# Kernel tuning notes

Measured on AMD Instinct MI355X. Metric: run time of the kernel, lower is better.

Reference implementation:

```python
import jax, jax.numpy as jnp
import numpy as np

N_CH = 62
B = 128
F = 32
T = 128
K = 3
HID = 512
OUT = 4
E_PER = 992


def setup_inputs() -> dict:
    key = jax.random.key(0)
    ks = jax.random.split(key, 16)
    N = B * N_CH
    E = B * E_PER
    x = jax.random.normal(ks[0], (N, F, T), dtype=jnp.float32)
    # one shared intra-graph edge pattern, offset per graph; no self-loops
    src0 = jax.random.randint(ks[1], (E_PER,), 0, N_CH)
    off = jax.random.randint(ks[2], (E_PER,), 1, N_CH)
    dst0 = (src0 + off) % N_CH
    gid = (jnp.arange(B) * N_CH)[:, None]
    src = (src0[None, :] + gid).reshape(-1)
    dst = (dst0[None, :] + gid).reshape(-1)
    edge_index = jnp.stack([src, dst]).astype(jnp.int32)
    edge_weight = jax.random.uniform(ks[3], (E,), dtype=jnp.float32, minval=0.1, maxval=1.0)
    batch = jnp.repeat(jnp.arange(B, dtype=jnp.int32), N_CH)
    sF = 1.0 / np.sqrt(F)
    sI = 1.0 / np.sqrt(N_CH * F)
    sH = 1.0 / np.sqrt(HID)
    return {
        'x': x, 'edge_index': edge_index, 'edge_weight': edge_weight, 'batch': batch,
        'W_cheb1': jax.random.normal(ks[4], (K, F, F), jnp.float32) * sF,
        'b_cheb1': jnp.zeros((F,), jnp.float32),
        'W_cheb2': jax.random.normal(ks[5], (K, F, F), jnp.float32) * sF,
        'b_cheb2': jnp.zeros((F,), jnp.float32),
        'W_ih': jax.random.normal(ks[6], (3 * HID, N_CH * F), jnp.float32) * sI,
        'W_hh': jax.random.normal(ks[7], (3 * HID, HID), jnp.float32) * sH,
        'b_ih': jnp.zeros((3 * HID,), jnp.float32),
        'b_hh': jnp.zeros((3 * HID,), jnp.float32),
        'W_lin': jax.random.normal(ks[8], (OUT, HID), jnp.float32) * sH,
        'b_lin': jnp.zeros((OUT,), jnp.float32),
    }


def _cheb_conv(x, src, dst, w, W, b):
    # PyG ChebConv, normalization='sym', lambda_max=2 => L_hat off-diag = -D^-1/2 A D^-1/2, diag 0
    N = x.shape[0]
    deg = jax.ops.segment_sum(w, src, num_segments=N)
    dinv = jnp.where(deg > 0, jax.lax.rsqrt(deg), 0.0)
    wn = -dinv[src] * w * dinv[dst]

    def prop(t):  # t: [N, F, T]
        return jax.ops.segment_sum(wn[:, None, None] * t[src], dst, num_segments=N)

    Tx0 = x
    out = jnp.einsum('nft,fg->ngt', Tx0, W[0])
    Tx1 = prop(Tx0)
    out = out + jnp.einsum('nft,fg->ngt', Tx1, W[1])
    for k in range(2, W.shape[0]):
        Tx2 = 2.0 * prop(Tx1) - Tx0
        out = out + jnp.einsum('nft,fg->ngt', Tx2, W[k])
        Tx0, Tx1 = Tx1, Tx2
    return out + b[None, :, None]


def _gru(seq, W_ih, W_hh, b_ih, b_hh):  # seq: [B, T, D]
    xg = jnp.einsum('btd,gd->btg', seq, W_ih) + b_ih  # [B, T, 3H] input gates precomputed
    h0 = jnp.zeros((seq.shape[0], W_hh.shape[1]), seq.dtype)

    def step(h, xg_t):
        hg = h @ W_hh.T + b_hh
        xr, xz, xn = jnp.split(xg_t, 3, axis=-1)
        hr, hz, hn = jnp.split(hg, 3, axis=-1)
        r = jax.nn.sigmoid(xr + hr)
        z = jax.nn.sigmoid(xz + hz)
        n = jnp.tanh(xn + r * hn)
        return (1.0 - z) * n + z * h, None

    hT, _ = jax.lax.scan(step, h0, jnp.swapaxes(xg, 0, 1))
    return hT  # [B, H]


def reference(x, edge_index, edge_weight, batch, W_cheb1, b_cheb1, W_cheb2, b_cheb2,
              W_ih, W_hh, b_ih, b_hh, W_lin, b_lin):
    src, dst = edge_index[0], edge_index[1]
    h = jax.nn.leaky_relu(_cheb_conv(x, src, dst, edge_weight, W_cheb1, b_cheb1), 0.01)
    h = _cheb_conv(h, src, dst, edge_weight, W_cheb2, b_cheb2)  # [N, F, T]
    nb = h.shape[0] // N_CH
    h = h.reshape(nb, N_CH * h.shape[1], h.shape[2])  # [B, 62F, T]
    h = jnp.swapaxes(h, 1, 2)  # [B, T, 62F]
    hid = _gru(h, W_ih, W_hh, b_ih, b_hh)  # dropout is identity (eval / p=0)
    return hid @ W_lin.T + b_lin
```

## Files before the change

kernel.cpp:

```cpp
#include <hip/hip_runtime.h>
#include <math.h>

#define N_CH 62
#define NB 128
#define F 32
#define TLEN 128
#define HID 512
#define G3 1536
#define EPER 992
#define NNODE (N_CH * NB)
#define ETOT (EPER * NB)
#define DIM (N_CH * F)
#define MROWS (NB * TLEN)
#define GRU_BLOCKS 16

typedef __attribute__((ext_vector_type(8))) short bf16x8;
typedef __attribute__((ext_vector_type(4))) float f32x4;

__device__ __forceinline__ unsigned short f2bf(float f) {
  unsigned u = __float_as_uint(f);
  unsigned r = u + 0x7fffu + ((u >> 16) & 1u);
  return (unsigned short)(r >> 16);
}
__device__ __forceinline__ float bf2f(unsigned short u) {
  return __uint_as_float(((unsigned)u) << 16);
}
__device__ __forceinline__ float sigmoidf_(float x) { return 1.f / (1.f + __expf(-x)); }

__device__ __forceinline__ void gl_lds16(const void* g, void* l) {
  __builtin_amdgcn_global_load_lds(
      (const __attribute__((address_space(1))) unsigned int*)g,
      (__attribute__((address_space(3))) unsigned int*)l, 16, 0, 0);
}

__global__ void k_deg(const int* __restrict__ src, const float* __restrict__ w,
                      float* __restrict__ deg) {
  int e = blockIdx.x * 256 + threadIdx.x;
  if (e < ETOT) atomicAdd(&deg[src[e]], w[e]);
}

__global__ void k_wn(const int* __restrict__ src, const int* __restrict__ dst,
                     const float* __restrict__ w, const float* __restrict__ deg,
                     float* __restrict__ wn) {
  int e = blockIdx.x * 256 + threadIdx.x;
  if (e < ETOT) {
    float ds = deg[src[e]], dd = deg[dst[e]];
    float a = ds > 0.f ? rsqrtf(ds) : 0.f;
    float b = dd > 0.f ? rsqrtf(dd) : 0.f;
    wn[e] = -a * w[e] * b;
  }
}

__global__ void k_ldense(const int* __restrict__ src, const int* __restrict__ dst,
                         const float* __restrict__ wn, float* __restrict__ Lf) {
  int e = blockIdx.x * 256 + threadIdx.x;
  if (e < ETOT) {
    int b = e / EPER;
    int s = src[e] - b * N_CH;
    int d = dst[e] - b * N_CH;
    atomicAdd(&Lf[(size_t)b * 4096 + d * 64 + s], wn[e]);
  }
}

__global__ __launch_bounds__(256) void k_m2(const float* __restrict__ Lf,
                                            unsigned short* __restrict__ Lbf,
                                            unsigned short* __restrict__ M2bf) {
  int b = blockIdx.x, tid = threadIdx.x;
  __shared__ float Ls[4096];
  for (int i = tid; i < 4096; i += 256) Ls[i] = Lf[(size_t)b * 4096 + i];
  __syncthreads();
  for (int h = 0; h < 16; h++) {
    int i = h * 256 + tid;
    int d = i >> 6, s = i & 63;
    float m = 0.f;
#pragma unroll 8
    for (int k = 0; k < 64; k++) m += Ls[d * 64 + k] * Ls[k * 64 + s];
    M2bf[(size_t)b * 4096 + i] = f2bf(2.f * m - (d == s ? 1.f : 0.f));
    Lbf[(size_t)b * 4096 + i] = f2bf(Ls[i]);
  }
}

__global__ __launch_bounds__(256) void k_xt(const float* __restrict__ x,
                                            unsigned short* __restrict__ Xt0) {
  int b = blockIdx.x >> 5, f = blockIdx.x & 31;
  int tid = threadIdx.x;
  for (int u = tid; u < 1024; u += 256) {
    int t = u >> 3, ch = u & 7;
    unsigned short o[8];
#pragma unroll
    for (int j = 0; j < 8; j++) {
      int n = ch * 8 + j;
      float v = (n < N_CH) ? x[((size_t)(b * N_CH + n) * F + f) * TLEN + t] : 0.f;
      o[j] = f2bf(v);
    }
    *(uint4*)&Xt0[((size_t)b * 4096 + t * 32 + f) * 64 + ch * 8] = *(uint4*)o;
  }
}

template <int LAYER>
__global__ __launch_bounds__(256) void k_cheb(const unsigned short* __restrict__ Xt,
                                              const unsigned short* __restrict__ Lbg,
                                              const unsigned short* __restrict__ M2g,
                                              const float* __restrict__ W,
                                              const float* __restrict__ bias,
                                              void* __restrict__ outv) {
  int b = blockIdx.x >> 5, ts = blockIdx.x & 31;
  int tid = threadIdx.x;
  int wid = tid >> 6, lane = tid & 63;
  int lr = lane & 15, lk = lane >> 4;
  __shared__ unsigned short Z0[128 * 64];
  __shared__ unsigned short P1[128 * 64];
  __shared__ unsigned short P2[128 * 64];

  const size_t tile_base = ((size_t)b * 4096 + ts * 128) * 64;

#pragma unroll
  for (int h = 0; h < 4; h++) {
    int p = h * 256 + tid;
    int row = p >> 3, c = (p & 7) ^ (row & 7);
    gl_lds16(Xt + tile_base + (size_t)row * 64 + c * 8,
             &Z0[(h * 256 + wid * 64) * 8]);
  }
  __syncthreads();

  f32x4 acc1[2][4], acc2[2][4];
#pragma unroll
  for (int mt = 0; mt < 2; mt++)
#pragma unroll
    for (int nt = 0; nt < 4; nt++) {
      acc1[mt][nt] = (f32x4){0.f, 0.f, 0.f, 0.f};
      acc2[mt][nt] = (f32x4){0.f, 0.f, 0.f, 0.f};
    }
  const unsigned short* Lbb = Lbg + (size_t)b * 4096;
  const unsigned short* Mbb = M2g + (size_t)b * 4096;
#pragma unroll
  for (int kk = 0; kk < 2; kk++) {
    bf16x8 af[2];
#pragma unroll
    for (int mt = 0; mt < 2; mt++) {
      int row = wid * 32 + mt * 16 + lr;
      af[mt] = *(const bf16x8*)&Z0[row * 64 + ((((kk << 2) + lk) ^ (row & 7)) << 3)];
    }
#pragma unroll
    for (int nt = 0; nt < 4; nt++) {
      int brow = nt * 16 + lr;
      bf16x8 bL = *(const bf16x8*)&Lbb[brow * 64 + kk * 32 + lk * 8];
      bf16x8 bM = *(const bf16x8*)&Mbb[brow * 64 + kk * 32 + lk * 8];
#pragma unroll
      for (int mt = 0; mt < 2; mt++) {
        acc1[mt][nt] = __builtin_amdgcn_mfma_f32_16x16x32_bf16(af[mt], bL, acc1[mt][nt], 0, 0, 0);
        acc2[mt][nt] = __builtin_amdgcn_mfma_f32_16x16x32_bf16(af[mt], bM, acc2[mt][nt], 0, 0, 0);
      }
    }
  }
#pragma unroll
  for (int mt = 0; mt < 2; mt++)
#pragma unroll
    for (int nt = 0; nt < 4; nt++) {
      int n = nt * 16 + lr;
#pragma unroll
      for (int r = 0; r < 4; r++) {
        int row = wid * 32 + mt * 16 + lk * 4 + r;
        int elem = row * 64 + ((((n >> 3) ^ (row & 7)) << 3)) + (n & 7);
        P1[elem] = f2bf(acc1[mt][nt][r]);
        P2[elem] = f2bf(acc2[mt][nt][r]);
      }
    }
  __syncthreads();

  int tl = tid >> 6, n = tid & 63;
  float acc[32];
#pragma unroll
  for (int g = 0; g < 32; g++) acc[g] = bias[g];
#pragma unroll 4
  for (int f = 0; f < 32; f++) {
    int row = tl * 32 + f;
    int elem = row * 64 + ((((n >> 3) ^ (row & 7)) << 3)) + (n & 7);
    float z0 = bf2f(Z0[elem]);
    float p1 = bf2f(P1[elem]);
    float p2 = bf2f(P2[elem]);
#pragma unroll
    for (int g = 0; g < 32; g++) {
      acc[g] += z0 * W[f * 32 + g] + p1 * W[1024 + f * 32 + g] + p2 * W[2048 + f * 32 + g];
    }
  }

  if (LAYER == 1) {
    unsigned short* out = (unsigned short*)outv;
    unsigned short* dst = out + tile_base + (size_t)(tl * 32) * 64 + n;
#pragma unroll
    for (int g = 0; g < 32; g++) {
      float y = acc[g];
      y = y > 0.f ? y : 0.01f * y;
      dst[g * 64] = f2bf(y);
    }
  } else {
    if (n < N_CH) {
      unsigned uu[16];
#pragma unroll
      for (int q = 0; q < 16; q++)
        uu[q] = (unsigned)f2bf(acc[2 * q]) | ((unsigned)f2bf(acc[2 * q + 1]) << 16);
      unsigned short* dst = (unsigned short*)outv +
                            ((size_t)(b * TLEN + ts * 4 + tl)) * DIM + n * F;
#pragma unroll
      for (int q = 0; q < 4; q++)
        *(uint4*)(dst + q * 8) = *(uint4*)&uu[q * 4];
    }
  }
}

__global__ void k_cvt(const float* __restrict__ in, unsigned short* __restrict__ out, int n) {
  int i = (blockIdx.x * 256 + threadIdx.x) * 4;
  if (i < n) {
    float4 v = *(const float4*)&in[i];
    ushort4 o;
    o.x = f2bf(v.x); o.y = f2bf(v.y); o.z = f2bf(v.z); o.w = f2bf(v.w);
    *(ushort4*)&out[i] = o;
  }
}

__global__ __launch_bounds__(256) void k_gemm_mfma(const unsigned short* __restrict__ Aq,
                                                   const unsigned short* __restrict__ Bq,
                                                   const float* __restrict__ bias,
                                                   float* __restrict__ Cmat) {
  __shared__ unsigned short As[4096];
  __shared__ unsigned short Bs[4096];
  int tid = threadIdx.x;
  int wid = tid >> 6, lane = tid & 63;
  int lr = lane & 15, lk = lane >> 4;
  int m0 = blockIdx.x * 128, n0 = blockIdx.y * 128;
  int wm = (wid & 1) * 64, wn = (wid >> 1) * 64;
  f32x4 zero = {0.f, 0.f, 0.f, 0.f};
  f32x4 acc[4][4];
#pragma unroll
  for (int i = 0; i < 4; i++)
#pragma unroll
    for (int j = 0; j < 4; j++) acc[i][j] = zero;

  int s0 = tid, s1 = tid + 256;
  const unsigned short* ga0 = Aq + (size_t)(m0 + (s0 >> 2)) * DIM + (s0 & 3) * 8;
  const unsigned short* ga1 = Aq + (size_t)(m0 + (s1 >> 2)) * DIM + (s1 & 3) * 8;
  const unsigned short* gb0 = Bq + (size_t)(n0 + (s0 >> 2)) * DIM + (s0 & 3) * 8;
  const unsigned short* gb1 = Bq + (size_t)(n0 + (s1 >> 2)) * DIM + (s1 & 3) * 8;

  for (int k0 = 0; k0 < DIM; k0 += 32) {
    gl_lds16(ga0 + k0, &As[wid * 512]);
    gl_lds16(ga1 + k0, &As[(wid + 4) * 512]);
    gl_lds16(gb0 + k0, &Bs[wid * 512]);
    gl_lds16(gb1 + k0, &Bs[(wid + 4) * 512]);
    __syncthreads();
    bf16x8 a[4], b[4];
#pragma unroll
    for (int mi = 0; mi < 4; mi++)
      a[mi] = *(const bf16x8*)&As[(wm + mi * 16 + lr) * 32 + lk * 8];
#pragma unroll
    for (int ni = 0; ni < 4; ni++)
      b[ni] = *(const bf16x8*)&Bs[(wn + ni * 16 + lr) * 32 + lk * 8];
#pragma unroll
    for (int mi = 0; mi < 4; mi++)
#pragma unroll
      for (int ni = 0; ni < 4; ni++)
        acc[mi][ni] = __builtin_amdgcn_mfma_f32_16x16x32_bf16(a[mi], b[ni], acc[mi][ni], 0, 0, 0);
    __syncthreads();
  }

#pragma unroll
  for (int mi = 0; mi < 4; mi++)
#pragma unroll
    for (int ni = 0; ni < 4; ni++) {
      int row = m0 + wm + mi * 16 + lk * 4;
      int col = n0 + wn + ni * 16 + lr;
      float bv = bias[col];
#pragma unroll
      for (int r = 0; r < 4; r++)
        Cmat[(size_t)(row + r) * G3 + col] = acc[mi][ni][r] + bv;
    }
}

#define LDH(I, OFFS) \
  asm volatile("global_load_dwordx4 %0, %1, off offset:" OFFS " sc0 sc1" \
               : "=v"(av[I]) : "v"(hin_p));
#define STH(VAL, OFFS) \
  asm volatile("global_store_short %0, %1, off offset:" OFFS " sc0 sc1" \
               :: "v"(hout_p), "v"((unsigned)(VAL)) : "memory");

__global__ __launch_bounds__(512, 1) void k_gru_persistent(
    const float* __restrict__ xg,
    const unsigned short* __restrict__ Wb,
    const float* __restrict__ bhh,
    unsigned short* __restrict__ hbA,
    unsigned short* __restrict__ hbB,
    float* __restrict__ hf_out,
    unsigned int* __restrict__ flags) {
  __shared__ unsigned short Wlds[96 * 520];
  int tid = threadIdx.x;
  int wv = tid >> 6, lane = tid & 63;
  int lr = lane & 15, lk = lane >> 4;
  int jh0 = blockIdx.x * 32;
  int mo = wv * 16;

  for (int i = tid; i < 96 * 64; i += 512) {
    int row = i >> 6, chunk = i & 63;
    int g = row >> 5, jj = row & 31;
    bf16x8 v = *(const bf16x8*)&Wb[(size_t)(g * HID + jh0 + jj) * HID + chunk * 8];
    *(bf16x8*)&Wlds[row * 520 + chunk * 8] = v;
  }
  __syncthreads();

  float br[2], bz[2], bn[2];
#pragma unroll
  for (int a = 0; a < 2; a++) {
    int j = jh0 + a * 16 + lr;
    br[a] = bhh[j]; bz[a] = bhh[HID + j]; bn[a] = bhh[2 * HID + j];
  }

  float hm[2][4];
#pragma unroll
  for (int a = 0; a < 2; a++)
#pragma unroll
    for (int r = 0; r < 4; r++) hm[a][r] = 0.f;

  float xv[2][4][3];
#pragma unroll
  for (int a = 0; a < 2; a++) {
    int j = jh0 + a * 16 + lr;
#pragma unroll
    for (int r = 0; r < 4; r++) {
      size_t xrow = ((size_t)(mo + lk * 4 + r) * TLEN + 0) * G3;
      xv[a][r][0] = xg[xrow + j];
      xv[a][r][1] = xg[xrow + HID + j];
      xv[a][r][2] = xg[xrow + 2 * HID + j];
    }
  }

  int fidx = (lane & 15) * 16;

  for (int t = 0; t < TLEN; t++) {
    const unsigned short* hin = (t & 1) ? hbB : hbA;
    unsigned short* hout = (t & 1) ? hbA : hbB;
    const unsigned short* hin_p = hin + (size_t)(mo + lr) * HID + lk * 8;
    unsigned short* hout_p = hout + (size_t)(mo + lk * 4) * HID + jh0 + lr;

    bf16x8 av[16];
    LDH(0, "0")    LDH(1, "64")   LDH(2, "128")  LDH(3, "192")
    LDH(4, "256")  LDH(5, "320")  LDH(6, "384")  LDH(7, "448")
    LDH(8, "512")  LDH(9, "576")  LDH(10, "640") LDH(11, "704")
    LDH(12, "768") LDH(13, "832") LDH(14, "896") LDH(15, "960")
    asm volatile("s_waitcnt vmcnt(0)" ::: "memory");
    __builtin_amdgcn_sched_barrier(0);

    f32x4 acc[6];
#pragma unroll
    for (int n = 0; n < 6; n++) acc[n] = (f32x4){0.f, 0.f, 0.f, 0.f};
#pragma unroll
    for (int ks = 0; ks < 16; ks++) {
#pragma unroll
      for (int n = 0; n < 6; n++) {
        bf16x8 bv = *(const bf16x8*)&Wlds[((n >> 1) * 32 + (n & 1) * 16 + lr) * 520 + ks * 32 + lk * 8];
        acc[n] = __builtin_amdgcn_mfma_f32_16x16x32_bf16(av[ks], bv, acc[n], 0, 0, 0);
      }
    }

    unsigned hv[2][4];
#pragma unroll
    for (int a = 0; a < 2; a++) {
#pragma unroll
      for (int r = 0; r < 4; r++) {
        float rr = sigmoidf_(xv[a][r][0] + acc[a][r] + br[a]);
        float zz = sigmoidf_(xv[a][r][1] + acc[2 + a][r] + bz[a]);
        float nn = tanhf(xv[a][r][2] + rr * (acc[4 + a][r] + bn[a]));
        float hnew = (1.f - zz) * nn + zz * hm[a][r];
        hm[a][r] = hnew;
        hv[a][r] = f2bf(hnew);
      }
    }

    STH(hv[0][0], "0")    STH(hv[0][1], "1024") STH(hv[0][2], "2048") STH(hv[0][3], "3072")
    STH(hv[1][0], "32")   STH(hv[1][1], "1056") STH(hv[1][2], "2080") STH(hv[1][3], "3104")

    if (t < TLEN - 1) {
      asm volatile("s_waitcnt vmcnt(0)" ::: "memory");
      __syncthreads();
      if (tid == 0)
        __hip_atomic_store(&flags[blockIdx.x * 16], (unsigned)(t + 1),
                           __ATOMIC_RELAXED, __HIP_MEMORY_SCOPE_AGENT);

      float xn[2][4][3];
#pragma unroll
      for (int a = 0; a < 2; a++) {
        int j = jh0 + a * 16 + lr;
#pragma unroll
        for (int r = 0; r < 4; r++) {
          size_t xrow = ((size_t)(mo + lk * 4 + r) * TLEN + (t + 1)) * G3;
          xn[a][r][0] = xg[xrow + j];
          xn[a][r][1] = xg[xrow + HID + j];
          xn[a][r][2] = xg[xrow + 2 * HID + j];
        }
      }

      unsigned tgt = (unsigned)(t + 1);
      while (true) {
        unsigned v = __hip_atomic_load(&flags[fidx], __ATOMIC_RELAXED, __HIP_MEMORY_SCOPE_AGENT);
        if (__ballot(v >= tgt) == ~0ull) break;
        __builtin_amdgcn_s_sleep(0);
      }

#pragma unroll
      for (int a = 0; a < 2; a++)
#pragma unroll
        for (int r = 0; r < 4; r++) {
          xv[a][r][0] = xn[a][r][0];
          xv[a][r][1] = xn[a][r][1];
          xv[a][r][2] = xn[a][r][2];
        }
    }
  }

#pragma unroll
  for (int a = 0; a < 2; a++)
#pragma unroll
    for (int r = 0; r < 4; r++)
      hf_out[(size_t)(mo + lk * 4 + r) * HID + jh0 + a * 16 + lr] = hm[a][r];
}

__global__ void k_final(const float* __restrict__ h, const float* __restrict__ Wlin,
                        const float* __restrict__ blin, float* __restrict__ out) {
  int b = blockIdx.x;
  int tid = threadIdx.x;
  int o = tid >> 6, lane = tid & 63;
  float acc = 0.f;
  for (int k = lane; k < HID; k += 64) acc += h[(size_t)b * HID + k] * Wlin[o * HID + k];
#pragma unroll
  for (int off = 32; off; off >>= 1) acc += __shfl_down(acc, off);
  if (lane == 0) out[b * 4 + o] = acc + blin[o];
}

extern "C" void kernel_launch(void* const* d_in, const int* in_sizes, int n_in,
                              void* d_out, int out_size, void* d_ws, size_t ws_size,
                              hipStream_t stream) {
  const float* x = (const float*)d_in[0];
  const int* eidx = (const int*)d_in[1];
  const float* ew = (const float*)d_in[2];
  const float* Wc1 = (const float*)d_in[4];
  const float* bc1 = (const float*)d_in[5];
  const float* Wc2 = (const float*)d_in[6];
  const float* bc2 = (const float*)d_in[7];
  const float* Wih = (const float*)d_in[8];
  const float* Whh = (const float*)d_in[9];
  const float* bih = (const float*)d_in[10];
  const float* bhh = (const float*)d_in[11];
  const float* Wlin = (const float*)d_in[12];
  const float* blin = (const float*)d_in[13];
  const int* src = eidx;
  const int* dst = eidx + ETOT;

  char* ws = (char*)d_ws;
  unsigned short* Xt0 = (unsigned short*)ws;
  unsigned short* Xt1 = (unsigned short*)(ws + 67108864);
  unsigned short* Db  = (unsigned short*)(ws + 134217728);
  float* xg = (float*)(ws + 199229440);
  char* S = ws + 299892736;
  float* deg = (float*)S;
  float* wn = (float*)(S + 32768);
  float* Lf = (float*)(S + 540672);
  unsigned short* Lb = (unsigned short*)(S + 2637824);
  unsigned short* M2b = (unsigned short*)(S + 3686400);
  unsigned short* Wihb = (unsigned short*)(S + 4734976);
  unsigned short* Whhb = (unsigned short*)(S + 10829824);
  float* hf = (float*)(S + 12402688);
  unsigned short* hbA = (unsigned short*)(S + 12664832);
  unsigned short* hbB = (unsigned short*)(S + 12795904);
  unsigned int* flags = (unsigned int*)(S + 12926976);

  if (ws_size < 312820736) return;

  hipMemsetAsync(deg, 0, 32768, stream);
  hipMemsetAsync(Lf, 0, 2097152, stream);
  hipMemsetAsync(hbA, 0, 131072, stream);
  hipMemsetAsync(flags, 0, 1024, stream);

  k_deg<<<ETOT / 256, 256, 0, stream>>>(src, ew, deg);
  k_wn<<<ETOT / 256, 256, 0, stream>>>(src, dst, ew, deg, wn);
  k_ldense<<<ETOT / 256, 256, 0, stream>>>(src, dst, wn, Lf);
  k_m2<<<NB, 256, 0, stream>>>(Lf, Lb, M2b);
  k_xt<<<NB * 32, 256, 0, stream>>>(x, Xt0);

  k_cheb<1><<<NB * 32, 256, 0, stream>>>(Xt0, Lb, M2b, Wc1, bc1, Xt1);
  k_cheb<2><<<NB * 32, 256, 0, stream>>>(Xt1, Lb, M2b, Wc2, bc2, Db);

  k_cvt<<<(G3 * DIM / 4 + 255) / 256, 256, 0, stream>>>(Wih, Wihb, G3 * DIM);
  k_cvt<<<(G3 * HID / 4 + 255) / 256, 256, 0, stream>>>(Whh, Whhb, G3 * HID);

  dim3 gg(MROWS / 128, G3 / 128);
  k_gemm_mfma<<<gg, 256, 0, stream>>>(Db, Wihb, bih, xg);

  k_gru_persistent<<<GRU_BLOCKS, 512, 0, stream>>>(xg, Whhb, bhh, hbA, hbB, hf, flags);

  k_final<<<NB, 256, 0, stream>>>(hf, Wlin, blin, (float*)d_out);
}
```

Before: 1.766 ms.

## Replace GRU flag barrier with per-element step tags and split K polling

```diff
diff --git a/kernel.cpp b/kernel.cpp
--- a/kernel.cpp
+++ b/kernel.cpp
@@ -16,6 +16,7 @@
 
 typedef __attribute__((ext_vector_type(8))) short bf16x8;
 typedef __attribute__((ext_vector_type(4))) float f32x4;
+typedef __attribute__((ext_vector_type(4))) unsigned int u32x4;
 
 __device__ __forceinline__ unsigned short f2bf(float f) {
   unsigned u = __float_as_uint(f);
@@ -31,6 +32,15 @@
   __builtin_amdgcn_global_load_lds(
       (const __attribute__((address_space(1))) unsigned int*)g,
       (__attribute__((address_space(3))) unsigned int*)l, 16, 0, 0);
+}
+
+__device__ __forceinline__ bf16x8 pack_hi(u32x4 lo, u32x4 hi) {
+  u32x4 r;
+  r[0] = (lo[0] >> 16) | (lo[1] & 0xffff0000u);
+  r[1] = (lo[2] >> 16) | (lo[3] & 0xffff0000u);
+  r[2] = (hi[0] >> 16) | (hi[1] & 0xffff0000u);
+  r[3] = (hi[2] >> 16) | (hi[3] & 0xffff0000u);
+  return __builtin_bit_cast(bf16x8, r);
 }
 
 __global__ void k_deg(const int* __restrict__ src, const float* __restrict__ w,
@@ -84,16 +94,29 @@
                                             unsigned short* __restrict__ Xt0) {
   int b = blockIdx.x >> 5, f = blockIdx.x & 31;
   int tid = threadIdx.x;
-  for (int u = tid; u < 1024; u += 256) {
-    int t = u >> 3, ch = u & 7;
-    unsigned short o[8];
-#pragma unroll
-    for (int j = 0; j < 8; j++) {
-      int n = ch * 8 + j;
-      float v = (n < N_CH) ? x[((size_t)(b * N_CH + n) * F + f) * TLEN + t] : 0.f;
-      o[j] = f2bf(v);
-    }
-    *(uint4*)&Xt0[((size_t)b * 4096 + t * 32 + f) * 64 + ch * 8] = *(uint4*)o;
+  __shared__ unsigned short T[128 * 72];
+#pragma unroll
+  for (int h = 0; h < 8; h++) {
+    int idx = h * 256 + tid;
+    int n = idx >> 5, tq = idx & 31;
+    if (n < N_CH) {
+      float4 v = *(const float4*)&x[(((size_t)(b * N_CH + n)) * F + f) * TLEN + tq * 4];
+      T[(tq * 4 + 0) * 72 + n] = f2bf(v.x);
+      T[(tq * 4 + 1) * 72 + n] = f2bf(v.y);
+      T[(tq * 4 + 2) * 72 + n] = f2bf(v.z);
+      T[(tq * 4 + 3) * 72 + n] = f2bf(v.w);
+    } else {
+      T[(tq * 4 + 0) * 72 + n] = 0; T[(tq * 4 + 1) * 72 + n] = 0;
+      T[(tq * 4 + 2) * 72 + n] = 0; T[(tq * 4 + 3) * 72 + n] = 0;
+    }
+  }
+  __syncthreads();
+  int t = tid >> 1, half = tid & 1;
+  unsigned short* dst = &Xt0[((size_t)b * 4096 + t * 32 + f) * 64 + half * 32];
+#pragma unroll
+  for (int q = 0; q < 4; q++) {
+    uint4 v = *(const uint4*)&T[t * 72 + half * 32 + q * 8];
+    *(uint4*)(dst + q * 8) = v;
   }
 }
 
@@ -277,21 +300,35 @@
     }
 }
 
-#define LDH(I, OFFS) \
-  asm volatile("global_load_dwordx4 %0, %1, off offset:" OFFS " sc0 sc1" \
-               : "=v"(av[I]) : "v"(hin_p));
-#define STH(VAL, OFFS) \
-  asm volatile("global_store_short %0, %1, off offset:" OFFS " sc0 sc1" \
-               :: "v"(hout_p), "v"((unsigned)(VAL)) : "memory");
+#define LDK(ARR, I, OFF) \
+  asm volatile("global_load_dwordx4 %0, %1, off offset:" OFF " sc0 sc1" \
+               : "=v"(ARR[I]) : "v"(hp));
+#define LD16_0 \
+  LDK(st, 0, "0")    LDK(st, 1, "16")   LDK(st, 2, "128")  LDK(st, 3, "144") \
+  LDK(st, 4, "256")  LDK(st, 5, "272")  LDK(st, 6, "384")  LDK(st, 7, "400") \
+  LDK(st, 8, "512")  LDK(st, 9, "528")  LDK(st, 10, "640") LDK(st, 11, "656") \
+  LDK(st, 12, "768") LDK(st, 13, "784") LDK(st, 14, "896") LDK(st, 15, "912")
+#define LD16_1 \
+  LDK(st, 0, "1024") LDK(st, 1, "1040") LDK(st, 2, "1152") LDK(st, 3, "1168") \
+  LDK(st, 4, "1280") LDK(st, 5, "1296") LDK(st, 6, "1408") LDK(st, 7, "1424") \
+  LDK(st, 8, "1536") LDK(st, 9, "1552") LDK(st, 10, "1664") LDK(st, 11, "1680") \
+  LDK(st, 12, "1792") LDK(st, 13, "1808") LDK(st, 14, "1920") LDK(st, 15, "1936")
+#define STW(P, VAL, OFF) \
+  asm volatile("global_store_dword %0, %1, off offset:" OFF " sc0 sc1" \
+               :: "v"(P), "v"(VAL) : "memory");
+#define TAGCHK \
+  unsigned diff = 0; \
+  _Pragma("unroll") \
+  for (int i_ = 0; i_ < 16; i_++) \
+    diff |= (st[i_][0] ^ tag) | (st[i_][1] ^ tag) | (st[i_][2] ^ tag) | (st[i_][3] ^ tag);
 
 __global__ __launch_bounds__(512, 1) void k_gru_persistent(
     const float* __restrict__ xg,
     const unsigned short* __restrict__ Wb,
     const float* __restrict__ bhh,
-    unsigned short* __restrict__ hbA,
-    unsigned short* __restrict__ hbB,
-    float* __restrict__ hf_out,
-    unsigned int* __restrict__ flags) {
+    unsigned* __restrict__ hA,
+    unsigned* __restrict__ hB,
+    float* __restrict__ hf_out) {
   __shared__ unsigned short Wlds[96 * 520];
   int tid = threadIdx.x;
   int wv = tid >> 6, lane = tid & 63;
@@ -333,35 +370,75 @@
     }
   }
 
-  int fidx = (lane & 15) * 16;
-
   for (int t = 0; t < TLEN; t++) {
-    const unsigned short* hin = (t & 1) ? hbB : hbA;
-    unsigned short* hout = (t & 1) ? hbA : hbB;
-    const unsigned short* hin_p = hin + (size_t)(mo + lr) * HID + lk * 8;
-    unsigned short* hout_p = hout + (size_t)(mo + lk * 4) * HID + jh0 + lr;
-
-    bf16x8 av[16];
-    LDH(0, "0")    LDH(1, "64")   LDH(2, "128")  LDH(3, "192")
-    LDH(4, "256")  LDH(5, "320")  LDH(6, "384")  LDH(7, "448")
-    LDH(8, "512")  LDH(9, "576")  LDH(10, "640") LDH(11, "704")
-    LDH(12, "768") LDH(13, "832") LDH(14, "896") LDH(15, "960")
-    asm volatile("s_waitcnt vmcnt(0)" ::: "memory");
-    __builtin_amdgcn_sched_barrier(0);
+    const unsigned* hin = (t & 1) ? hB : hA;
+    unsigned* hout = (t & 1) ? hA : hB;
+    const unsigned* hp = hin + (size_t)(mo + lr) * HID + lk * 8;
+    unsigned tag = (unsigned)t;
+
+    u32x4 st[16];
+    bf16x8 av0[8];
+
+    LD16_0;
+    for (;;) {
+      asm volatile("s_waitcnt vmcnt(0)" ::: "memory");
+      __builtin_amdgcn_sched_barrier(0);
+      TAGCHK
+      if (__all((int)((diff & 0xffffu) == 0))) break;
+      LD16_0;
+    }
+#pragma unroll
+    for (int q = 0; q < 8; q++) av0[q] = pack_hi(st[2 * q], st[2 * q + 1]);
+
+    LD16_1;
 
     f32x4 acc[6];
 #pragma unroll
     for (int n = 0; n < 6; n++) acc[n] = (f32x4){0.f, 0.f, 0.f, 0.f};
 #pragma unroll
-    for (int ks = 0; ks < 16; ks++) {
+    for (int q = 0; q < 8; q++) {
 #pragma unroll
       for (int n = 0; n < 6; n++) {
-        bf16x8 bv = *(const bf16x8*)&Wlds[((n >> 1) * 32 + (n & 1) * 16 + lr) * 520 + ks * 32 + lk * 8];
-        acc[n] = __builtin_amdgcn_mfma_f32_16x16x32_bf16(av[ks], bv, acc[n], 0, 0, 0);
-      }
-    }
-
-    unsigned hv[2][4];
+        bf16x8 bv = *(const bf16x8*)&Wlds[((n >> 1) * 32 + (n & 1) * 16 + lr) * 520 + q * 32 + lk * 8];
+        acc[n] = __builtin_amdgcn_mfma_f32_16x16x32_bf16(av0[q], bv, acc[n], 0, 0, 0);
+      }
+    }
+
+    for (;;) {
+      asm volatile("s_waitcnt vmcnt(0)" ::: "memory");
+      __builtin_amdgcn_sched_barrier(0);
+      TAGCHK
+      if (__all((int)((diff & 0xffffu) == 0))) break;
+      LD16_1;
+    }
+
+    float xn[2][4][3];
+    {
+      int tp = (t + 1 < TLEN) ? t + 1 : t;
+#pragma unroll
+      for (int a = 0; a < 2; a++) {
+        int j = jh0 + a * 16 + lr;
+#pragma unroll
+        for (int r = 0; r < 4; r++) {
+          size_t xrow = ((size_t)(mo + lk * 4 + r) * TLEN + tp) * G3;
+          xn[a][r][0] = xg[xrow + j];
+          xn[a][r][1] = xg[xrow + HID + j];
+          xn[a][r][2] = xg[xrow + 2 * HID + j];
+        }
+      }
+    }
+
+#pragma unroll
+    for (int q = 0; q < 8; q++) {
+      bf16x8 av = pack_hi(st[2 * q], st[2 * q + 1]);
+#pragma unroll
+      for (int n = 0; n < 6; n++) {
+        bf16x8 bv = *(const bf16x8*)&Wlds[((n >> 1) * 32 + (n & 1) * 16 + lr) * 520 + (8 + q) * 32 + lk * 8];
+        acc[n] = __builtin_amdgcn_mfma_f32_16x16x32_bf16(av, bv, acc[n], 0, 0, 0);
+      }
+    }
+
+    unsigned w_[2][4];
 #pragma unroll
     for (int a = 0; a < 2; a++) {
 #pragma unroll
@@ -371,49 +448,27 @@
         float nn = tanhf(xv[a][r][2] + rr * (acc[4 + a][r] + bn[a]));
         float hnew = (1.f - zz) * nn + zz * hm[a][r];
         hm[a][r] = hnew;
-        hv[a][r] = f2bf(hnew);
-      }
-    }
-
-    STH(hv[0][0], "0")    STH(hv[0][1], "1024") STH(hv[0][2], "2048") STH(hv[0][3], "3072")
-    STH(hv[1][0], "32")   STH(hv[1][1], "1056") STH(hv[1][2], "2080") STH(hv[1][3], "3104")
+        w_[a][r] = ((unsigned)f2bf(hnew) << 16) | (unsigned)(t + 1);
+      }
+    }
 
     if (t < TLEN - 1) {
-      asm volatile("s_waitcnt vmcnt(0)" ::: "memory");
-      __syncthreads();
-      if (tid == 0)
-        __hip_atomic_store(&flags[blockIdx.x * 16], (unsigned)(t + 1),
-                           __ATOMIC_RELAXED, __HIP_MEMORY_SCOPE_AGENT);
-
-      float xn[2][4][3];
-#pragma unroll
-      for (int a = 0; a < 2; a++) {
-        int j = jh0 + a * 16 + lr;
-#pragma unroll
-        for (int r = 0; r < 4; r++) {
-          size_t xrow = ((size_t)(mo + lk * 4 + r) * TLEN + (t + 1)) * G3;
-          xn[a][r][0] = xg[xrow + j];
-          xn[a][r][1] = xg[xrow + HID + j];
-          xn[a][r][2] = xg[xrow + 2 * HID + j];
-        }
-      }
-
-      unsigned tgt = (unsigned)(t + 1);
-      while (true) {
-        unsigned v = __hip_atomic_load(&flags[fidx], __ATOMIC_RELAXED, __HIP_MEMORY_SCOPE_AGENT);
-        if (__ballot(v >= tgt) == ~0ull) break;
-        __builtin_amdgcn_s_sleep(0);
-      }
-
-#pragma unroll
-      for (int a = 0; a < 2; a++)
-#pragma unroll
-        for (int r = 0; r < 4; r++) {
-          xv[a][r][0] = xn[a][r][0];
-          xv[a][r][1] = xn[a][r][1];
-          xv[a][r][2] = xn[a][r][2];
-        }
-    }
+      unsigned* hop = hout + (size_t)(mo + lk * 4) * HID + jh0 + lr;
+      unsigned* hop2 = hop + 2 * HID;
+      STW(hop,  w_[0][0], "0")    STW(hop,  w_[0][1], "2048")
+      STW(hop2, w_[0][2], "0")    STW(hop2, w_[0][3], "2048")
+      STW(hop,  w_[1][0], "64")   STW(hop,  w_[1][1], "2112")
+      STW(hop2, w_[1][2], "64")   STW(hop2, w_[1][3], "2112")
+    }
+
+#pragma unroll
+    for (int a = 0; a < 2; a++)
+#pragma unroll
+      for (int r = 0; r < 4; r++) {
+        xv[a][r][0] = xn[a][r][0];
+        xv[a][r][1] = xn[a][r][1];
+        xv[a][r][2] = xn[a][r][2];
+      }
   }
 
 #pragma unroll
@@ -468,16 +523,15 @@
   unsigned short* Wihb = (unsigned short*)(S + 4734976);
   unsigned short* Whhb = (unsigned short*)(S + 10829824);
   float* hf = (float*)(S + 12402688);
-  unsigned short* hbA = (unsigned short*)(S + 12664832);
-  unsigned short* hbB = (unsigned short*)(S + 12795904);
-  unsigned int* flags = (unsigned int*)(S + 12926976);
-
-  if (ws_size < 312820736) return;
+  unsigned* hA32 = (unsigned*)(S + 12664832);
+  unsigned* hB32 = (unsigned*)(S + 12926976);
+
+  if (ws_size < 313081856) return;
 
   hipMemsetAsync(deg, 0, 32768, stream);
   hipMemsetAsync(Lf, 0, 2097152, stream);
-  hipMemsetAsync(hbA, 0, 131072, stream);
-  hipMemsetAsync(flags, 0, 1024, stream);
+  hipMemsetAsync(hA32, 0, 262144, stream);
+  hipMemsetAsync(hB32, 0, 262144, stream);
 
   k_deg<<<ETOT / 256, 256, 0, stream>>>(src, ew, deg);
   k_wn<<<ETOT / 256, 256, 0, stream>>>(src, dst, ew, deg, wn);
@@ -494,7 +548,7 @@
   dim3 gg(MROWS / 128, G3 / 128);
   k_gemm_mfma<<<gg, 256, 0, stream>>>(Db, Wihb, bih, xg);
 
-  k_gru_persistent<<<GRU_BLOCKS, 512, 0, stream>>>(xg, Whhb, bhh, hbA, hbB, hf, flags);
+  k_gru_persistent<<<GRU_BLOCKS, 512, 0, stream>>>(xg, Whhb, bhh, hA32, hB32, hf);
 
   k_final<<<NB, 256, 0, stream>>>(hf, Wlin, blin, (float*)d_out);
 }
```

Result: slower. 2.197 ms (+24.4%).

## Fuse input-gate GEMM into persistent GRU kernel with per-timestep readiness counters

Applied to the files above, without the earlier changes.

```diff
diff --git a/kernel.cpp b/kernel.cpp
--- a/kernel.cpp
+++ b/kernel.cpp
@@ -12,6 +12,7 @@
 #define ETOT (EPER * NB)
 #define DIM (N_CH * F)
 #define MROWS (NB * TLEN)
+#define GEMM_BLOCKS 192
 #define GRU_BLOCKS 16
 
 typedef __attribute__((ext_vector_type(8))) short bf16x8;
@@ -84,16 +85,29 @@
                                             unsigned short* __restrict__ Xt0) {
   int b = blockIdx.x >> 5, f = blockIdx.x & 31;
   int tid = threadIdx.x;
-  for (int u = tid; u < 1024; u += 256) {
-    int t = u >> 3, ch = u & 7;
-    unsigned short o[8];
-#pragma unroll
-    for (int j = 0; j < 8; j++) {
-      int n = ch * 8 + j;
-      float v = (n < N_CH) ? x[((size_t)(b * N_CH + n) * F + f) * TLEN + t] : 0.f;
-      o[j] = f2bf(v);
-    }
-    *(uint4*)&Xt0[((size_t)b * 4096 + t * 32 + f) * 64 + ch * 8] = *(uint4*)o;
+  __shared__ unsigned short T[128 * 72];
+#pragma unroll
+  for (int h = 0; h < 8; h++) {
+    int idx = h * 256 + tid;
+    int n = idx >> 5, tq = idx & 31;
+    if (n < N_CH) {
+      float4 v = *(const float4*)&x[(((size_t)(b * N_CH + n)) * F + f) * TLEN + tq * 4];
+      T[(tq * 4 + 0) * 72 + n] = f2bf(v.x);
+      T[(tq * 4 + 1) * 72 + n] = f2bf(v.y);
+      T[(tq * 4 + 2) * 72 + n] = f2bf(v.z);
+      T[(tq * 4 + 3) * 72 + n] = f2bf(v.w);
+    } else {
+      T[(tq * 4 + 0) * 72 + n] = 0; T[(tq * 4 + 1) * 72 + n] = 0;
+      T[(tq * 4 + 2) * 72 + n] = 0; T[(tq * 4 + 3) * 72 + n] = 0;
+    }
+  }
+  __syncthreads();
+  int t = tid >> 1, half = tid & 1;
+  unsigned short* dst = &Xt0[((size_t)b * 4096 + t * 32 + f) * 64 + half * 32];
+#pragma unroll
+  for (int q = 0; q < 4; q++) {
+    uint4 v = *(const uint4*)&T[t * 72 + half * 32 + q * 8];
+    *(uint4*)(dst + q * 8) = v;
   }
 }
 
@@ -201,7 +215,7 @@
       for (int q = 0; q < 16; q++)
         uu[q] = (unsigned)f2bf(acc[2 * q]) | ((unsigned)f2bf(acc[2 * q + 1]) << 16);
       unsigned short* dst = (unsigned short*)outv +
-                            ((size_t)(b * TLEN + ts * 4 + tl)) * DIM + n * F;
+                            ((size_t)(ts * 4 + tl) * NB + b) * DIM + n * F;
 #pragma unroll
       for (int q = 0; q < 4; q++)
         *(uint4*)(dst + q * 8) = *(uint4*)&uu[q * 4];
@@ -219,90 +233,99 @@
   }
 }
 
-__global__ __launch_bounds__(256) void k_gemm_mfma(const unsigned short* __restrict__ Aq,
-                                                   const unsigned short* __restrict__ Bq,
-                                                   const float* __restrict__ bias,
-                                                   float* __restrict__ Cmat) {
-  __shared__ unsigned short As[4096];
-  __shared__ unsigned short Bs[4096];
-  int tid = threadIdx.x;
-  int wid = tid >> 6, lane = tid & 63;
-  int lr = lane & 15, lk = lane >> 4;
-  int m0 = blockIdx.x * 128, n0 = blockIdx.y * 128;
-  int wm = (wid & 1) * 64, wn = (wid >> 1) * 64;
-  f32x4 zero = {0.f, 0.f, 0.f, 0.f};
-  f32x4 acc[4][4];
-#pragma unroll
-  for (int i = 0; i < 4; i++)
-#pragma unroll
-    for (int j = 0; j < 4; j++) acc[i][j] = zero;
-
-  int s0 = tid, s1 = tid + 256;
-  const unsigned short* ga0 = Aq + (size_t)(m0 + (s0 >> 2)) * DIM + (s0 & 3) * 8;
-  const unsigned short* ga1 = Aq + (size_t)(m0 + (s1 >> 2)) * DIM + (s1 & 3) * 8;
-  const unsigned short* gb0 = Bq + (size_t)(n0 + (s0 >> 2)) * DIM + (s0 & 3) * 8;
-  const unsigned short* gb1 = Bq + (size_t)(n0 + (s1 >> 2)) * DIM + (s1 & 3) * 8;
-
-  for (int k0 = 0; k0 < DIM; k0 += 32) {
-    gl_lds16(ga0 + k0, &As[wid * 512]);
-    gl_lds16(ga1 + k0, &As[(wid + 4) * 512]);
-    gl_lds16(gb0 + k0, &Bs[wid * 512]);
-    gl_lds16(gb1 + k0, &Bs[(wid + 4) * 512]);
-    __syncthreads();
-    bf16x8 a[4], b[4];
-#pragma unroll
-    for (int mi = 0; mi < 4; mi++)
-      a[mi] = *(const bf16x8*)&As[(wm + mi * 16 + lr) * 32 + lk * 8];
-#pragma unroll
-    for (int ni = 0; ni < 4; ni++)
-      b[ni] = *(const bf16x8*)&Bs[(wn + ni * 16 + lr) * 32 + lk * 8];
-#pragma unroll
-    for (int mi = 0; mi < 4; mi++)
-#pragma unroll
-      for (int ni = 0; ni < 4; ni++)
-        acc[mi][ni] = __builtin_amdgcn_mfma_f32_16x16x32_bf16(a[mi], b[ni], acc[mi][ni], 0, 0, 0);
-    __syncthreads();
-  }
-
-#pragma unroll
-  for (int mi = 0; mi < 4; mi++)
-#pragma unroll
-    for (int ni = 0; ni < 4; ni++) {
-      int row = m0 + wm + mi * 16 + lk * 4;
-      int col = n0 + wn + ni * 16 + lr;
-      float bv = bias[col];
-#pragma unroll
-      for (int r = 0; r < 4; r++)
-        Cmat[(size_t)(row + r) * G3 + col] = acc[mi][ni][r] + bv;
-    }
-}
-
 #define LDH(I, OFFS) \
   asm volatile("global_load_dwordx4 %0, %1, off offset:" OFFS " sc0 sc1" \
                : "=v"(av[I]) : "v"(hin_p));
 #define STH(VAL, OFFS) \
   asm volatile("global_store_short %0, %1, off offset:" OFFS " sc0 sc1" \
                :: "v"(hout_p), "v"((unsigned)(VAL)) : "memory");
-
-__global__ __launch_bounds__(512, 1) void k_gru_persistent(
-    const float* __restrict__ xg,
-    const unsigned short* __restrict__ Wb,
+#define STC(P, VAL) \
+  asm volatile("global_store_dword %0, %1, off sc0 sc1" \
+               :: "v"(P), "v"(VAL) : "memory");
+
+__global__ __launch_bounds__(512, 1) void k_fused(
+    const unsigned short* __restrict__ seq,
+    const unsigned short* __restrict__ Wihb,
+    const float* __restrict__ bih,
+    float* __restrict__ xg,
+    unsigned int* __restrict__ cnt,
+    const unsigned short* __restrict__ Whhb,
     const float* __restrict__ bhh,
     unsigned short* __restrict__ hbA,
     unsigned short* __restrict__ hbB,
     float* __restrict__ hf_out,
     unsigned int* __restrict__ flags) {
+  __shared__ unsigned short As[4096];
+  __shared__ unsigned short Bs[4096];
   __shared__ unsigned short Wlds[96 * 520];
   int tid = threadIdx.x;
   int wv = tid >> 6, lane = tid & 63;
   int lr = lane & 15, lk = lane >> 4;
-  int jh0 = blockIdx.x * 32;
+
+  if (blockIdx.x < GEMM_BLOCKS) {
+    int wm2 = wv & 1, wn4 = wv >> 1;
+    for (int s = 0; s < 8; s++) {
+      int tile = blockIdx.x + GEMM_BLOCKS * s;
+      int mt = tile / 12, nt = tile % 12;
+      int m0 = mt * 128, n0 = nt * 128;
+      f32x4 acc[4][2];
+#pragma unroll
+      for (int i = 0; i < 4; i++)
+#pragma unroll
+        for (int j = 0; j < 2; j++) acc[i][j] = (f32x4){0.f, 0.f, 0.f, 0.f};
+
+      const unsigned short* ga = seq + (size_t)(m0 + (tid >> 2)) * DIM + (tid & 3) * 8;
+      const unsigned short* gb = Wihb + (size_t)(n0 + (tid >> 2)) * DIM + (tid & 3) * 8;
+      for (int k0 = 0; k0 < DIM; k0 += 32) {
+        __syncthreads();
+        gl_lds16(ga + k0, &As[wv * 512]);
+        gl_lds16(gb + k0, &Bs[wv * 512]);
+        __syncthreads();
+        bf16x8 a[4], b[2];
+#pragma unroll
+        for (int mi = 0; mi < 4; mi++)
+          a[mi] = *(const bf16x8*)&As[(wm2 * 64 + mi * 16 + lr) * 32 + lk * 8];
+#pragma unroll
+        for (int ni = 0; ni < 2; ni++)
+          b[ni] = *(const bf16x8*)&Bs[(wn4 * 32 + ni * 16 + lr) * 32 + lk * 8];
+#pragma unroll
+        for (int mi = 0; mi < 4; mi++)
+#pragma unroll
+          for (int ni = 0; ni < 2; ni++)
+            acc[mi][ni] = __builtin_amdgcn_mfma_f32_16x16x32_bf16(a[mi], b[ni], acc[mi][ni], 0, 0, 0);
+      }
+      float bv[2];
+      bv[0] = bih[n0 + wn4 * 32 + lr];
+      bv[1] = bih[n0 + wn4 * 32 + 16 + lr];
+#pragma unroll
+      for (int mi = 0; mi < 4; mi++)
+#pragma unroll
+        for (int ni = 0; ni < 2; ni++) {
+          int col = n0 + wn4 * 32 + ni * 16 + lr;
+          int row0 = m0 + wm2 * 64 + mi * 16 + lk * 4;
+#pragma unroll
+          for (int r = 0; r < 4; r++) {
+            float v = acc[mi][ni][r] + bv[ni];
+            float* p = xg + (size_t)(row0 + r) * G3 + col;
+            STC(p, v)
+          }
+        }
+      asm volatile("s_waitcnt vmcnt(0)" ::: "memory");
+      __syncthreads();
+      if (tid == 0)
+        __hip_atomic_fetch_add(&cnt[mt], 1u, __ATOMIC_RELAXED, __HIP_MEMORY_SCOPE_AGENT);
+    }
+    return;
+  }
+
+  int jb = blockIdx.x - GEMM_BLOCKS;
+  int jh0 = jb * 32;
   int mo = wv * 16;
 
   for (int i = tid; i < 96 * 64; i += 512) {
     int row = i >> 6, chunk = i & 63;
     int g = row >> 5, jj = row & 31;
-    bf16x8 v = *(const bf16x8*)&Wb[(size_t)(g * HID + jh0 + jj) * HID + chunk * 8];
+    bf16x8 v = *(const bf16x8*)&Whhb[(size_t)(g * HID + jh0 + jj) * HID + chunk * 8];
     *(bf16x8*)&Wlds[row * 520 + chunk * 8] = v;
   }
   __syncthreads();
@@ -320,13 +343,15 @@
 #pragma unroll
     for (int r = 0; r < 4; r++) hm[a][r] = 0.f;
 
+  while (__hip_atomic_load(&cnt[0], __ATOMIC_RELAXED, __HIP_MEMORY_SCOPE_AGENT) < 12u)
+    __builtin_amdgcn_s_sleep(1);
   float xv[2][4][3];
 #pragma unroll
   for (int a = 0; a < 2; a++) {
     int j = jh0 + a * 16 + lr;
 #pragma unroll
     for (int r = 0; r < 4; r++) {
-      size_t xrow = ((size_t)(mo + lk * 4 + r) * TLEN + 0) * G3;
+      size_t xrow = (size_t)(mo + lk * 4 + r) * G3;
       xv[a][r][0] = xg[xrow + j];
       xv[a][r][1] = xg[xrow + HID + j];
       xv[a][r][2] = xg[xrow + 2 * HID + j];
@@ -382,8 +407,11 @@
       asm volatile("s_waitcnt vmcnt(0)" ::: "memory");
       __syncthreads();
       if (tid == 0)
-        __hip_atomic_store(&flags[blockIdx.x * 16], (unsigned)(t + 1),
+        __hip_atomic_store(&flags[jb * 16], (unsigned)(t + 1),
                            __ATOMIC_RELAXED, __HIP_MEMORY_SCOPE_AGENT);
+
+      while (__hip_atomic_load(&cnt[t + 1], __ATOMIC_RELAXED, __HIP_MEMORY_SCOPE_AGENT) < 12u)
+        __builtin_amdgcn_s_sleep(1);
 
       float xn[2][4][3];
 #pragma unroll
@@ -391,7 +419,7 @@
         int j = jh0 + a * 16 + lr;
 #pragma unroll
         for (int r = 0; r < 4; r++) {
-          size_t xrow = ((size_t)(mo + lk * 4 + r) * TLEN + (t + 1)) * G3;
+          size_t xrow = ((size_t)(t + 1) * NB + mo + lk * 4 + r) * G3;
           xn[a][r][0] = xg[xrow + j];
           xn[a][r][1] = xg[xrow + HID + j];
           xn[a][r][2] = xg[xrow + 2 * HID + j];
@@ -471,13 +499,15 @@
   unsigned short* hbA = (unsigned short*)(S + 12664832);
   unsigned short* hbB = (unsigned short*)(S + 12795904);
   unsigned int* flags = (unsigned int*)(S + 12926976);
-
-  if (ws_size < 312820736) return;
+  unsigned int* cnt = (unsigned int*)(S + 12928000);
+
+  if (ws_size < 312821248) return;
 
   hipMemsetAsync(deg, 0, 32768, stream);
   hipMemsetAsync(Lf, 0, 2097152, stream);
   hipMemsetAsync(hbA, 0, 131072, stream);
   hipMemsetAsync(flags, 0, 1024, stream);
+  hipMemsetAsync(cnt, 0, 512, stream);
 
   k_deg<<<ETOT / 256, 256, 0, stream>>>(src, ew, deg);
   k_wn<<<ETOT / 256, 256, 0, stream>>>(src, dst, ew, deg, wn);
@@ -491,10 +521,8 @@
   k_cvt<<<(G3 * DIM / 4 + 255) / 256, 256, 0, stream>>>(Wih, Wihb, G3 * DIM);
   k_cvt<<<(G3 * HID / 4 + 255) / 256, 256, 0, stream>>>(Whh, Whhb, G3 * HID);
 
-  dim3 gg(MROWS / 128, G3 / 128);
-  k_gemm_mfma<<<gg, 256, 0, stream>>>(Db, Wihb, bih, xg);
-
-  k_gru_persistent<<<GRU_BLOCKS, 512, 0, stream>>>(xg, Whhb, bhh, hbA, hbB, hf, flags);
+  k_fused<<<GEMM_BLOCKS + GRU_BLOCKS, 512, 0, stream>>>(
+      Db, Wihb, bih, xg, cnt, Whhb, bhh, hbA, hbB, hf, flags);
 
   k_final<<<NB, 256, 0, stream>>>(hf, Wlin, blin, (float*)d_out);
 }
```

Result: no change. 1.765 ms (-0.1%).
